# Kernel tuning notes

Hardware: AMD Instinct MI355X
Metric: run time of the kernel (lower is better)

Reference implementation:

```python
import jax, jax.numpy as jnp
import numpy as np

ALPHA = 1.0
STRIDE = 1
PAD = 1
DIL = 1


def setup_inputs() -> dict:
    key = jax.random.key(0)
    k1, k2, k3, k4 = jax.random.split(key, 4)
    B, C_in, C_out, H, W, K = 8, 64, 64, 128, 128, 3
    n = C_in * K * K
    stdv = 1.0 / np.sqrt(n)
    x = jax.random.normal(k1, (B, C_in, H, W), dtype=jnp.float32)
    depth = jax.random.uniform(k2, (B, 1, H, W), dtype=jnp.float32)
    weight = jax.random.uniform(k3, (C_out, C_in, K, K), dtype=jnp.float32,
                                minval=-stdv, maxval=stdv)
    bias = jax.random.uniform(k4, (C_out,), dtype=jnp.float32,
                              minval=-stdv, maxval=stdv)
    return {"x": x, "depth": depth, "weight": weight, "bias": bias}


def reference(x, depth, weight, bias):
    # Depth-guided convolution:
    #   out[b,o,p0] = bias[o] + sum_{c,k} W[o,c,k] * x[b,c,p0+pk] * exp(-alpha*|D(p0)-D(p0+pk)|)
    B, C, H, W = x.shape
    O, _, KH, KW = weight.shape
    H_out = (H + 2 * PAD - (DIL * (KH - 1) + 1)) // STRIDE + 1
    W_out = (W + 2 * PAD - (DIL * (KW - 1) + 1)) // STRIDE + 1
    x_p = jnp.pad(x, ((0, 0), (0, 0), (PAD, PAD), (PAD, PAD)))
    d_p = jnp.pad(depth, ((0, 0), (0, 0), (PAD, PAD), (PAD, PAD)))

    def tap(a, kh, kw):
        h0, w0 = kh * DIL, kw * DIL
        return a[:, :, h0:h0 + (H_out - 1) * STRIDE + 1:STRIDE,
                 w0:w0 + (W_out - 1) * STRIDE + 1:STRIDE]

    # depth at the center of each receptive field (kernel assumed odd)
    d_center = tap(d_p, KH // 2, KW // 2)  # [B,1,Ho,Wo]

    out = jnp.zeros((B, O, H_out, W_out), dtype=x.dtype)
    for kh in range(KH):
        for kw in range(KW):
            xs = tap(x_p, kh, kw)                                  # [B,C,Ho,Wo]
            ds = tap(d_p, kh, kw)                                  # [B,1,Ho,Wo]
            sim = jnp.exp(-ALPHA * jnp.abs(ds - d_center))         # [B,1,Ho,Wo]
            out = out + jnp.einsum('oc,bchw->bohw', weight[:, :, kh, kw], xs * sim)
    return out + bias[None, :, None, None]
```

## Files before the change

### kernel.cpp

```cpp
#include <hip/hip_runtime.h>

#define B_ 8
#define C_ 64
#define O_ 64
#define H_ 128
#define W_ 128

typedef __attribute__((ext_vector_type(8))) short bf16x8;
typedef __attribute__((ext_vector_type(4))) float f32x4;

__device__ __forceinline__ unsigned short f2bf(float v) {
    unsigned u = __float_as_uint(v);
    return (unsigned short)((u + 0x7FFFu + ((u >> 16) & 1u)) >> 16);
}

__device__ __forceinline__ int swz(int col) {
    return ((col ^ (col >> 3)) & 7) << 4;
}

__global__ void prep_weights(const float* __restrict__ weight,
                             unsigned short* __restrict__ wfrag) {
    int idx = blockIdx.x * 256 + threadIdx.x;
    if (idx >= 9 * 4096) return;
    int j  = idx & 7;
    int l  = (idx >> 3) & 63;
    int fi = (idx >> 9) & 3;
    int ks = (idx >> 11) & 1;
    int t  = idx >> 12;
    int o  = fi * 16 + (l & 15);
    int c  = ks * 32 + ((l >> 4) & 3) * 8 + j;
    wfrag[idx] = f2bf(weight[(o * C_ + c) * 9 + t]);
}

__global__ __launch_bounds__(256, 2)
void depthconv_mfma4(const float* __restrict__ x,
                     const float* __restrict__ depth,
                     const unsigned short* __restrict__ wfrag,
                     const float* __restrict__ bias,
                     float* __restrict__ out) {
    __shared__ __align__(16) unsigned char xs[396 * 128];
    __shared__ __align__(16) float sim[9][4][64];
    __shared__ __align__(16) float dt[6][68];

    const int tid = threadIdx.x;
    const int blk = blockIdx.x;
    const int b   = blk >> 6;
    const int rem = blk & 63;
    const int h0  = (rem >> 1) * 4;
    const int w0  = (rem & 1) * 64;

    for (int i = tid; i < 396; i += 256) {
        int r = i / 66, col = i - r * 66;
        int gh = h0 - 1 + r, gw = w0 - 1 + col;
        bool ok = ((unsigned)gh < (unsigned)H_) && ((unsigned)gw < (unsigned)W_);
        int ghc = gh < 0 ? 0 : (gh > H_ - 1 ? H_ - 1 : gh);
        int gwc = gw < 0 ? 0 : (gw > W_ - 1 ? W_ - 1 : gw);
        float v = depth[(b * H_ + ghc) * W_ + gwc];
        dt[r][col] = ok ? v : 0.f;
    }
    __syncthreads();

    const int crb = tid >> 4;
    const int q   = tid & 15;
    float4 xv[24];
    #pragma unroll
    for (int k = 0; k < 24; ++k) {
        int idx = crb + 16 * k;
        int c = idx & 63, r = idx >> 6;
        int gh  = h0 - 1 + r;
        int ghc = gh < 0 ? 0 : (gh > H_ - 1 ? H_ - 1 : gh);
        xv[k] = *(const float4*)&x[((b * C_ + c) * H_ + ghc) * W_ + w0 + q * 4];
    }
    float hv[3];
    #pragma unroll
    for (int k = 0; k < 3; ++k) {
        int i = tid + 256 * k;
        int side = i & 1, cr = i >> 1;
        int c = cr & 63, r = cr >> 6;
        int gh = h0 - 1 + r;
        int gw = side ? (w0 + 64) : (w0 - 1);
        bool ok = ((unsigned)gh < (unsigned)H_) && ((unsigned)gw < (unsigned)W_);
        int ghc = gh < 0 ? 0 : (gh > H_ - 1 ? H_ - 1 : gh);
        int gwc = gw < 0 ? 0 : (gw > W_ - 1 ? W_ - 1 : gw);
        float v = x[((b * C_ + c) * H_ + ghc) * W_ + gwc];
        hv[k] = ok ? v : 0.f;
    }

    {
        int hr = (tid >> 6) & 3, px = tid & 63;
        float dc = dt[hr + 1][px + 1];
        #pragma unroll
        for (int t = 0; t < 9; ++t) {
            const int kh = t / 3, kw = t % 3;
            sim[t][hr][px] = expf(-fabsf(dt[hr + kh][px + kw] - dc));
        }
    }

    #pragma unroll
    for (int k = 0; k < 24; ++k) {
        int idx = crb + 16 * k;
        int c = idx & 63, r = idx >> 6;
        int gh = h0 - 1 + r;
        bool okh = (unsigned)gh < (unsigned)H_;
        float vv[4] = {xv[k].x, xv[k].y, xv[k].z, xv[k].w};
        #pragma unroll
        for (int m = 0; m < 4; ++m) {
            int col = 1 + q * 4 + m;
            int rc  = r * 66 + col;
            unsigned short bv = okh ? f2bf(vv[m]) : (unsigned short)0;
            *(unsigned short*)(xs + rc * 128 + ((2 * c) ^ swz(col))) = bv;
        }
    }
    #pragma unroll
    for (int k = 0; k < 3; ++k) {
        int i = tid + 256 * k;
        int side = i & 1, cr = i >> 1;
        int c = cr & 63, r = cr >> 6;
        int col = side ? 65 : 0;
        int rc  = r * 66 + col;
        *(unsigned short*)(xs + rc * 128 + ((2 * c) ^ swz(col))) = f2bf(hv[k]);
    }
    __syncthreads();

    const int lane = tid & 63;
    const int hr   = tid >> 6;
    const int g    = lane >> 4;
    const int ln   = lane & 15;

    float acc[4][4][4];
    #pragma unroll
    for (int of = 0; of < 4; ++of) {
        float bv = bias[of * 16 + ln];
        #pragma unroll
        for (int pf = 0; pf < 4; ++pf)
            #pragma unroll
            for (int r = 0; r < 4; ++r)
                acc[pf][of][r] = bv;
    }

    #pragma unroll 1
    for (int kh = 0; kh < 3; ++kh) {
        #pragma unroll
        for (int kw = 0; kw < 3; ++kw) {
            const int t = kh * 3 + kw;
            bf16x8 bfr[2][4];
            #pragma unroll
            for (int ks = 0; ks < 2; ++ks)
                #pragma unroll
                for (int of = 0; of < 4; ++of)
                    bfr[ks][of] = *(const bf16x8*)(
                        wfrag + (((t * 2 + ks) * 4 + of) * 64 + lane) * 8);

            #pragma unroll
            for (int pf = 0; pf < 4; ++pf) {
                int col = pf * 16 + ln + kw;
                int rcb = (hr + kh) * 66 + col;
                const unsigned char* rowp = xs + rcb * 128;
                bf16x8 af0 = *(const bf16x8*)(rowp + ((2 * (g * 8))      ^ swz(col)));
                bf16x8 af1 = *(const bf16x8*)(rowp + ((2 * (32 + g * 8)) ^ swz(col)));

                f32x4 prt[4] = {};
                #pragma unroll
                for (int of = 0; of < 4; ++of)
                    prt[of] = __builtin_amdgcn_mfma_f32_16x16x32_bf16(
                        af0, bfr[0][of], prt[of], 0, 0, 0);
                #pragma unroll
                for (int of = 0; of < 4; ++of)
                    prt[of] = __builtin_amdgcn_mfma_f32_16x16x32_bf16(
                        af1, bfr[1][of], prt[of], 0, 0, 0);

                f32x4 sv = *(const f32x4*)&sim[t][hr][pf * 16 + g * 4];
                #pragma unroll
                for (int of = 0; of < 4; ++of)
                    #pragma unroll
                    for (int r = 0; r < 4; ++r)
                        acc[pf][of][r] = fmaf(sv[r], prt[of][r], acc[pf][of][r]);
            }
        }
    }

    const int h = h0 + hr;
    #pragma unroll
    for (int of = 0; of < 4; ++of) {
        int o = of * 16 + ln;
        float* dst = out + (((size_t)(b * O_ + o) * H_ + h) * W_) + w0;
        #pragma unroll
        for (int pf = 0; pf < 4; ++pf) {
            f32x4 v = { acc[pf][of][0], acc[pf][of][1],
                        acc[pf][of][2], acc[pf][of][3] };
            *(f32x4*)(dst + pf * 16 + g * 4) = v;
        }
    }
}

extern "C" void kernel_launch(void* const* d_in, const int* in_sizes, int n_in,
                              void* d_out, int out_size, void* d_ws, size_t ws_size,
                              hipStream_t stream) {
    const float* x      = (const float*)d_in[0];
    const float* depth  = (const float*)d_in[1];
    const float* weight = (const float*)d_in[2];
    const float* bias   = (const float*)d_in[3];
    float* out          = (float*)d_out;
    unsigned short* wfrag = (unsigned short*)d_ws;

    prep_weights<<<dim3(144), dim3(256), 0, stream>>>(weight, wfrag);
    depthconv_mfma4<<<dim3(512), dim3(256), 0, stream>>>(
        x, depth, wfrag, bias, out);
}
```

Measured before the change: 37.07 us.

## Split output channels across two waves per row with 512-thread blocks

Doubles the block to 512 threads so each output row is handled by two waves, each computing half of the output channels. This halves the per-thread accumulators and MFMA count and should allow higher occupancy (launch bounds 512,4). The x staging now loads channel pairs and writes packed bf16x2 values into shared memory, halving LDS store instructions. The trade-off is that each wave re-reads the same A fragments from LDS, doubling LDS read traffic for activations.

Result: slower. 43.17 us (+16.5%).

```diff
diff --git a/kernel.cpp b/kernel.cpp
--- a/kernel.cpp
+++ b/kernel.cpp
@@ -1,10 +1,12 @@
 #include <hip/hip_runtime.h>
+#include <hip/hip_bf16.h>
 
 #define B_ 8
 #define C_ 64
 #define O_ 64
 #define H_ 128
 #define W_ 128
+#define HW_ (H_ * W_)
 
 typedef __attribute__((ext_vector_type(8))) short bf16x8;
 typedef __attribute__((ext_vector_type(4))) float f32x4;
@@ -13,9 +15,11 @@
     unsigned u = __float_as_uint(v);
     return (unsigned short)((u + 0x7FFFu + ((u >> 16) & 1u)) >> 16);
 }
-
 __device__ __forceinline__ int swz(int col) {
     return ((col ^ (col >> 3)) & 7) << 4;
+}
+__device__ __forceinline__ int clampi(int v, int lo, int hi) {
+    return v < lo ? lo : (v > hi ? hi : v);
 }
 
 __global__ void prep_weights(const float* __restrict__ weight,
@@ -32,12 +36,12 @@
     wfrag[idx] = f2bf(weight[(o * C_ + c) * 9 + t]);
 }
 
-__global__ __launch_bounds__(256, 2)
-void depthconv_mfma4(const float* __restrict__ x,
-                     const float* __restrict__ depth,
-                     const unsigned short* __restrict__ wfrag,
-                     const float* __restrict__ bias,
-                     float* __restrict__ out) {
+__global__ __launch_bounds__(512, 4)
+void depthconv_mfma10(const float* __restrict__ x,
+                      const float* __restrict__ depth,
+                      const unsigned short* __restrict__ wfrag,
+                      const float* __restrict__ bias,
+                      float* __restrict__ out) {
     __shared__ __align__(16) unsigned char xs[396 * 128];
     __shared__ __align__(16) float sim[9][4][64];
     __shared__ __align__(16) float dt[6][68];
@@ -49,88 +53,80 @@
     const int h0  = (rem >> 1) * 4;
     const int w0  = (rem & 1) * 64;
 
-    for (int i = tid; i < 396; i += 256) {
-        int r = i / 66, col = i - r * 66;
+    if (tid < 396) {
+        int r = tid / 66, col = tid - r * 66;
         int gh = h0 - 1 + r, gw = w0 - 1 + col;
         bool ok = ((unsigned)gh < (unsigned)H_) && ((unsigned)gw < (unsigned)W_);
-        int ghc = gh < 0 ? 0 : (gh > H_ - 1 ? H_ - 1 : gh);
-        int gwc = gw < 0 ? 0 : (gw > W_ - 1 ? W_ - 1 : gw);
-        float v = depth[(b * H_ + ghc) * W_ + gwc];
+        float v = depth[(b * H_ + clampi(gh, 0, H_ - 1)) * W_ + clampi(gw, 0, W_ - 1)];
         dt[r][col] = ok ? v : 0.f;
     }
     __syncthreads();
 
-    const int crb = tid >> 4;
-    const int q   = tid & 15;
-    float4 xv[24];
-    #pragma unroll
-    for (int k = 0; k < 24; ++k) {
-        int idx = crb + 16 * k;
-        int c = idx & 63, r = idx >> 6;
-        int gh  = h0 - 1 + r;
-        int ghc = gh < 0 ? 0 : (gh > H_ - 1 ? H_ - 1 : gh);
-        xv[k] = *(const float4*)&x[((b * C_ + c) * H_ + ghc) * W_ + w0 + q * 4];
-    }
-    float hv[3];
-    #pragma unroll
-    for (int k = 0; k < 3; ++k) {
-        int i = tid + 256 * k;
-        int side = i & 1, cr = i >> 1;
-        int c = cr & 63, r = cr >> 6;
-        int gh = h0 - 1 + r;
-        int gw = side ? (w0 + 64) : (w0 - 1);
+    const int q  = tid & 15;
+    const int pc = tid >> 4;
+    float4 xa[6], xb[6];
+    #pragma unroll
+    for (int r = 0; r < 6; ++r) {
+        int ghc = clampi(h0 - 1 + r, 0, H_ - 1);
+        const float* p = &x[((b * C_ + 2 * pc) * H_ + ghc) * W_ + w0 + q * 4];
+        xa[r] = *(const float4*)p;
+        xb[r] = *(const float4*)(p + HW_);
+    }
+    float hl0 = 0.f, hl1 = 0.f;
+    int hside = 0, hpair = 0, hrr = 0;
+    if (tid < 384) {
+        hside = tid & 1; hpair = (tid >> 1) & 31; hrr = tid >> 6;
+        int gh = h0 - 1 + hrr;
+        int gw = hside ? (w0 + 64) : (w0 - 1);
         bool ok = ((unsigned)gh < (unsigned)H_) && ((unsigned)gw < (unsigned)W_);
-        int ghc = gh < 0 ? 0 : (gh > H_ - 1 ? H_ - 1 : gh);
-        int gwc = gw < 0 ? 0 : (gw > W_ - 1 ? W_ - 1 : gw);
-        float v = x[((b * C_ + c) * H_ + ghc) * W_ + gwc];
-        hv[k] = ok ? v : 0.f;
-    }
-
-    {
-        int hr = (tid >> 6) & 3, px = tid & 63;
-        float dc = dt[hr + 1][px + 1];
-        #pragma unroll
-        for (int t = 0; t < 9; ++t) {
-            const int kh = t / 3, kw = t % 3;
-            sim[t][hr][px] = expf(-fabsf(dt[hr + kh][px + kw] - dc));
-        }
-    }
-
-    #pragma unroll
-    for (int k = 0; k < 24; ++k) {
-        int idx = crb + 16 * k;
-        int c = idx & 63, r = idx >> 6;
+        const float* p = &x[((b * C_ + 2 * hpair) * H_ + clampi(gh, 0, H_ - 1)) * W_
+                            + clampi(gw, 0, W_ - 1)];
+        float v0 = p[0], v1 = p[HW_];
+        hl0 = ok ? v0 : 0.f;
+        hl1 = ok ? v1 : 0.f;
+    }
+
+    for (int i = tid; i < 2304; i += 512) {
+        int t = i >> 8, sr = (i >> 6) & 3, px = i & 63;
+        int kh = t / 3, kw = t - kh * 3;
+        sim[t][sr][px] = expf(-fabsf(dt[sr + kh][px + kw] - dt[sr + 1][px + 1]));
+    }
+
+    #pragma unroll
+    for (int r = 0; r < 6; ++r) {
         int gh = h0 - 1 + r;
         bool okh = (unsigned)gh < (unsigned)H_;
-        float vv[4] = {xv[k].x, xv[k].y, xv[k].z, xv[k].w};
+        float va[4] = {xa[r].x, xa[r].y, xa[r].z, xa[r].w};
+        float vb[4] = {xb[r].x, xb[r].y, xb[r].z, xb[r].w};
         #pragma unroll
         for (int m = 0; m < 4; ++m) {
             int col = 1 + q * 4 + m;
-            int rc  = r * 66 + col;
-            unsigned short bv = okh ? f2bf(vv[m]) : (unsigned short)0;
-            *(unsigned short*)(xs + rc * 128 + ((2 * c) ^ swz(col))) = bv;
+            float2 pr;
+            pr.x = okh ? va[m] : 0.f;
+            pr.y = okh ? vb[m] : 0.f;
+            __hip_bfloat162 bv = __float22bfloat162_rn(pr);
+            *(__hip_bfloat162*)(xs + (r * 66 + col) * 128 + ((4 * pc) ^ swz(col))) = bv;
         }
     }
-    #pragma unroll
-    for (int k = 0; k < 3; ++k) {
-        int i = tid + 256 * k;
-        int side = i & 1, cr = i >> 1;
-        int c = cr & 63, r = cr >> 6;
-        int col = side ? 65 : 0;
-        int rc  = r * 66 + col;
-        *(unsigned short*)(xs + rc * 128 + ((2 * c) ^ swz(col))) = f2bf(hv[k]);
+    if (tid < 384) {
+        int col = hside ? 65 : 0;
+        float2 pr; pr.x = hl0; pr.y = hl1;
+        __hip_bfloat162 bv = __float22bfloat162_rn(pr);
+        *(__hip_bfloat162*)(xs + (hrr * 66 + col) * 128 + ((4 * hpair) ^ swz(col))) = bv;
     }
     __syncthreads();
 
     const int lane = tid & 63;
-    const int hr   = tid >> 6;
+    const int wv   = tid >> 6;
+    const int hr   = wv >> 1;
+    const int oh   = wv & 1;
     const int g    = lane >> 4;
     const int ln   = lane & 15;
 
-    float acc[4][4][4];
-    #pragma unroll
-    for (int of = 0; of < 4; ++of) {
-        float bv = bias[of * 16 + ln];
+    float acc[4][2][4];
+    #pragma unroll
+    for (int of = 0; of < 2; ++of) {
+        float bv = bias[(oh * 2 + of) * 16 + ln];
         #pragma unroll
         for (int pf = 0; pf < 4; ++pf)
             #pragma unroll
@@ -143,35 +139,36 @@
         #pragma unroll
         for (int kw = 0; kw < 3; ++kw) {
             const int t = kh * 3 + kw;
-            bf16x8 bfr[2][4];
+            bf16x8 bfr[2][2];
             #pragma unroll
             for (int ks = 0; ks < 2; ++ks)
                 #pragma unroll
-                for (int of = 0; of < 4; ++of)
+                for (int of = 0; of < 2; ++of) {
+                    int fi = oh * 2 + of;
                     bfr[ks][of] = *(const bf16x8*)(
-                        wfrag + (((t * 2 + ks) * 4 + of) * 64 + lane) * 8);
+                        wfrag + (((t * 2 + ks) * 4 + fi) * 64 + lane) * 8);
+                }
 
             #pragma unroll
             for (int pf = 0; pf < 4; ++pf) {
                 int col = pf * 16 + ln + kw;
-                int rcb = (hr + kh) * 66 + col;
-                const unsigned char* rowp = xs + rcb * 128;
-                bf16x8 af0 = *(const bf16x8*)(rowp + ((2 * (g * 8))      ^ swz(col)));
-                bf16x8 af1 = *(const bf16x8*)(rowp + ((2 * (32 + g * 8)) ^ swz(col)));
-
-                f32x4 prt[4] = {};
-                #pragma unroll
-                for (int of = 0; of < 4; ++of)
+                const unsigned char* rowp = xs + ((hr + kh) * 66 + col) * 128;
+                bf16x8 af0 = *(const bf16x8*)(rowp + ((16 * g) ^ swz(col)));
+                bf16x8 af1 = *(const bf16x8*)(rowp + ((64 + 16 * g) ^ swz(col)));
+
+                f32x4 prt[2] = {};
+                #pragma unroll
+                for (int of = 0; of < 2; ++of)
                     prt[of] = __builtin_amdgcn_mfma_f32_16x16x32_bf16(
                         af0, bfr[0][of], prt[of], 0, 0, 0);
                 #pragma unroll
-                for (int of = 0; of < 4; ++of)
+                for (int of = 0; of < 2; ++of)
                     prt[of] = __builtin_amdgcn_mfma_f32_16x16x32_bf16(
                         af1, bfr[1][of], prt[of], 0, 0, 0);
 
                 f32x4 sv = *(const f32x4*)&sim[t][hr][pf * 16 + g * 4];
                 #pragma unroll
-                for (int of = 0; of < 4; ++of)
+                for (int of = 0; of < 2; ++of)
                     #pragma unroll
                     for (int r = 0; r < 4; ++r)
                         acc[pf][of][r] = fmaf(sv[r], prt[of][r], acc[pf][of][r]);
@@ -181,8 +178,8 @@
 
     const int h = h0 + hr;
     #pragma unroll
-    for (int of = 0; of < 4; ++of) {
-        int o = of * 16 + ln;
+    for (int of = 0; of < 2; ++of) {
+        int o = (oh * 2 + of) * 16 + ln;
         float* dst = out + (((size_t)(b * O_ + o) * H_ + h) * W_) + w0;
         #pragma unroll
         for (int pf = 0; pf < 4; ++pf) {
@@ -204,6 +201,6 @@
     unsigned short* wfrag = (unsigned short*)d_ws;
 
     prep_weights<<<dim3(144), dim3(256), 0, stream>>>(weight, wfrag);
-    depthconv_mfma4<<<dim3(512), dim3(256), 0, stream>>>(
+    depthconv_mfma10<<<dim3(512), dim3(512), 0, stream>>>(
         x, depth, wfrag, bias, out);
 }
```
